# Kernel tuning notes

Measured on AMD Instinct MI355X. Metric: run time of the kernel, lower is better.

Reference implementation:

```python
import jax, jax.numpy as jnp
import numpy as np

N, FEAT, D, K, L, H, NCLS = 4096, 512, 64, 100, 3, 8, 2
EPS = 1e-15

def _ln(x, g, b, eps=1e-6):
    m = x.mean(-1, keepdims=True)
    v = x.var(-1, keepdims=True)
    return (x - m) * jax.lax.rsqrt(v + eps) * g + b


def setup_inputs():
    key = jax.random.key(0)
    ks = jax.random.split(key, 12)
    w = lambda k, shape: jax.random.normal(k, shape, jnp.float32) * 0.02
    return {
        "node_feat": jax.random.normal(ks[0], (1, N, FEAT), jnp.float32),
        "adj": jax.random.uniform(ks[1], (1, N, N), jnp.float32),
        "conv_w": w(ks[2], (FEAT, D)), "conv_b": jnp.zeros((D,), jnp.float32),
        "bn_g": jnp.ones((D,), jnp.float32), "bn_b": jnp.zeros((D,), jnp.float32),
        "pool_w": w(ks[3], (D, K)), "pool_b": jnp.zeros((K,), jnp.float32),
        "cls_token": jnp.zeros((1, 1, D), jnp.float32),
        "ln1_g": jnp.ones((L, D), jnp.float32), "ln1_b": jnp.zeros((L, D), jnp.float32),
        "qkv_w": w(ks[4], (L, D, 3 * D)), "qkv_b": jnp.zeros((L, 3 * D), jnp.float32),
        "proj_w": w(ks[5], (L, D, D)), "proj_b": jnp.zeros((L, D), jnp.float32),
        "ln2_g": jnp.ones((L, D), jnp.float32), "ln2_b": jnp.zeros((L, D), jnp.float32),
        "fc1_w": w(ks[6], (L, D, 4 * D)), "fc1_b": jnp.zeros((L, 4 * D), jnp.float32),
        "fc2_w": w(ks[7], (L, 4 * D, D)), "fc2_b": jnp.zeros((L, D), jnp.float32),
        "norm_g": jnp.ones((D,), jnp.float32), "norm_b": jnp.zeros((D,), jnp.float32),
        "head_w": w(ks[8], (D, NCLS)), "head_b": jnp.zeros((NCLS,), jnp.float32),
    }


def _forward(node_feat, adj, conv_w, conv_b, bn_g, bn_b, pool_w, pool_b, cls_token,
             ln1_g, ln1_b, qkv_w, qkv_b, proj_w, proj_b, ln2_g, ln2_b,
             fc1_w, fc1_b, fc2_w, fc2_b, norm_g, norm_b, head_w, head_b):
    x = node_feat  # mask is all ones -> X = mask*X is a no-op
    # --- GCNBlock: propagate + self loop + linear + BatchNorm(train stats) + L2 norm ---
    y = jnp.matmul(adj, x) + x                 # [1,N,F]
    y = y @ conv_w + conv_b                    # [1,N,D]
    m = y.mean(axis=(0, 1))
    v = y.var(axis=(0, 1))
    y = (y - m) * jax.lax.rsqrt(v + 1e-5) * bn_g + bn_b
    y = y / jnp.maximum(jnp.linalg.norm(y, axis=2, keepdims=True), 1e-12)
    # --- cluster assignment ---
    s = jax.nn.softmax(y @ pool_w + pool_b, axis=-1)   # [1,N,K]
    # --- dense_mincut_pool ---
    out = jnp.einsum('bnk,bnd->bkd', s, y)             # [1,K,D]
    sa = s[0].T @ adj[0]                               # [K,N] (the torch.sparse.mm)
    out_adj = (sa @ s[0])[None]                        # [1,K,K]
    mincut_num = jnp.trace(out_adj, axis1=1, axis2=2)  # [1]
    d_flat = adj.sum(-1)                               # [1,N] degrees
    # trace(S^T diag(d) S) = sum_i d_i * ||s_i||^2
    mincut_den = jnp.sum(d_flat[0] * jnp.sum(s[0] ** 2, axis=-1))[None]
    mincut_loss = jnp.mean(-(mincut_num / mincut_den))
    ss = jnp.einsum('bnk,bnl->bkl', s, s)
    i_s = jnp.eye(K, dtype=ss.dtype)
    ortho_loss = jnp.mean(jnp.linalg.norm(
        ss / jnp.linalg.norm(ss, axis=(-1, -2), keepdims=True) - i_s / jnp.linalg.norm(i_s),
        axis=(-1, -2)))
    ind = jnp.arange(K)
    out_adj = out_adj.at[:, ind, ind].set(0.0)
    dd = jnp.sqrt(out_adj.sum(-1))[:, None] + EPS      # [1,1,K]
    out_adj = out_adj / dd / jnp.swapaxes(dd, 1, 2)    # (returned by pool; unused downstream)
    # --- transformer over [cls] + K cluster tokens ---
    t = jnp.concatenate([jnp.broadcast_to(cls_token, (1, 1, D)), out], axis=1)  # [1,K+1,D]
    hd = D // H
    scale = hd ** -0.5
    for l in range(L):
        h = _ln(t, ln1_g[l], ln1_b[l])
        qkv = h @ qkv_w[l] + qkv_b[l]
        q, k, vv = jnp.split(qkv, 3, axis=-1)
        sp = lambda a: a.reshape(1, -1, H, hd).transpose(0, 2, 1, 3)
        q, k, vv = sp(q), sp(k), sp(vv)
        att = jax.nn.softmax(jnp.einsum('bhqd,bhkd->bhqk', q, k) * scale, axis=-1)
        o = jnp.einsum('bhqk,bhkd->bhqd', att, vv).transpose(0, 2, 1, 3).reshape(1, -1, D)
        t = t + (o @ proj_w[l] + proj_b[l])
        h = _ln(t, ln2_g[l], ln2_b[l])
        t = t + (jax.nn.gelu(h @ fc1_w[l] + fc1_b[l], approximate=False) @ fc2_w[l] + fc2_b[l])
    t = _ln(t, norm_g, norm_b)
    logits = t[:, 0] @ head_w + head_b                 # [1,NCLS]
    return logits, mincut_loss, ortho_loss


def reference(node_feat, adj, conv_w, conv_b, bn_g, bn_b, pool_w, pool_b, cls_token,
              ln1_g, ln1_b, qkv_w, qkv_b, proj_w, proj_b, ln2_g, ln2_b,
              fc1_w, fc1_b, fc2_w, fc2_b, norm_g, norm_b, head_w, head_b):
    return _forward(node_feat, adj, conv_w, conv_b, bn_g, bn_b, pool_w, pool_b, cls_token,
                    ln1_g, ln1_b, qkv_w, qkv_b, proj_w, proj_b, ln2_g, ln2_b,
                    fc1_w, fc1_b, fc2_w, fc2_b, norm_g, norm_b, head_w, head_b)
```

## Files before the change

kernel.cpp:

```cpp
#include <hip/hip_runtime.h>
#include <hip/hip_bf16.h>
#include <math.h>

#define NN   4096
#define FEAT 512
#define DIM  64
#define KC   100
#define LL   3

#define OFF_DFLAT   0
#define OFF_CHSUM   4096
#define OFF_CHSQ    4160
#define ZERO_FLOATS 4224
#define OFF_XW      4224
#define OFF_XWPART  (OFF_XW + NN*DIM)
#define OFF_GPART   OFF_XWPART
#define OFF_YPART   (OFF_XWPART + 8*NN*DIM)
#define OFF_Y0      (OFF_YPART + 8*NN*DIM)
#define OFF_TBUF    (OFF_Y0 + NN*DIM)
#define OFF_QKV     (OFF_TBUF + 101*DIM)
#define OFF_SS      (OFF_QKV + 101*192)
#define OFF_DENP    (OFF_SS + KC*KC)
#define OFF_NUMP    (OFF_DENP + 1024)
#define OFF_SB16    (OFF_NUMP + 1024)
#define OFF_STB16   (OFF_SB16 + NN*128/2)
#define OFF_YNT16   (OFF_STB16 + NN*128/2)
#define OFF_XWT16   (OFF_YNT16 + NN*DIM/2)

typedef __attribute__((ext_vector_type(8))) short bfrag;
typedef __attribute__((ext_vector_type(4))) float ffrag;

__device__ __forceinline__ unsigned short f2bf(float f) {
    union { float f; unsigned u; } v; v.f = f;
    return (unsigned short)((v.u + 0x7FFFu + ((v.u >> 16) & 1u)) >> 16);
}
__device__ __forceinline__ float bf2f(unsigned short u) {
    union { unsigned u; float f; } v; v.u = (unsigned)u << 16; return v.f;
}
__device__ __forceinline__ unsigned int pk2(float a, float b) {
    __hip_bfloat162 h = __float22bfloat162_rn(make_float2(a, b));
    return *(unsigned int*)&h;
}

__device__ __forceinline__ float wsum(float v) {
#pragma unroll
    for (int o = 32; o > 0; o >>= 1) v += __shfl_xor(v, o, 64);
    return v;
}
__device__ __forceinline__ float wmax(float v) {
#pragma unroll
    for (int o = 32; o > 0; o >>= 1) v = fmaxf(v, __shfl_xor(v, o, 64));
    return v;
}
__device__ __forceinline__ float hsum32(float v) {
#pragma unroll
    for (int o = 16; o > 0; o >>= 1) v += __shfl_xor(v, o, 64);
    return v;
}
__device__ __forceinline__ float hmax32(float v) {
#pragma unroll
    for (int o = 16; o > 0; o >>= 1) v = fmaxf(v, __shfl_xor(v, o, 64));
    return v;
}

template<int KDIM>
__global__ __launch_bounds__(256) void mm64(const float* __restrict__ A,
                                            const float* __restrict__ B,
                                            float* __restrict__ outp) {
    __shared__ float a_sh[64 * 68];
    __shared__ float b_sh[64 * 68];
    const int t  = threadIdx.x;
    const int rb = blockIdx.x;
    const int kspan = KDIM / gridDim.y;
    const int k0 = blockIdx.y * kspan;
    const int cg = t & 15, rg = t >> 4;
    const int srow = t >> 2, sq = t & 3;
    float4 acc[4];
#pragma unroll
    for (int i = 0; i < 4; ++i) acc[i] = make_float4(0.f, 0.f, 0.f, 0.f);
    const float* arow = A + (size_t)(rb * 64 + srow) * KDIM + k0;
    const float* brow = B + (size_t)(k0 + srow) * DIM;
    for (int kt = 0; kt < kspan; kt += 64) {
#pragma unroll
        for (int k = 0; k < 4; ++k) {
            const int j = sq * 4 + 16 * k;
            *(float4*)&a_sh[srow * 68 + j] = *(const float4*)(arow + kt + j);
            *(float4*)&b_sh[srow * 68 + j] = *(const float4*)(brow + (size_t)kt * DIM + j);
        }
        __syncthreads();
#pragma unroll 4
        for (int jj = 0; jj < 64; jj += 4) {
            const float4 w0 = *(float4*)&b_sh[(jj + 0) * 68 + 4 * cg];
            const float4 w1 = *(float4*)&b_sh[(jj + 1) * 68 + 4 * cg];
            const float4 w2 = *(float4*)&b_sh[(jj + 2) * 68 + 4 * cg];
            const float4 w3 = *(float4*)&b_sh[(jj + 3) * 68 + 4 * cg];
#pragma unroll
            for (int i = 0; i < 4; ++i) {
                const float4 av = *(float4*)&a_sh[(4 * rg + i) * 68 + jj];
                acc[i].x += av.x * w0.x + av.y * w1.x + av.z * w2.x + av.w * w3.x;
                acc[i].y += av.x * w0.y + av.y * w1.y + av.z * w2.y + av.w * w3.y;
                acc[i].z += av.x * w0.z + av.y * w1.z + av.z * w2.z + av.w * w3.z;
                acc[i].w += av.x * w0.w + av.y * w1.w + av.z * w2.w + av.w * w3.w;
            }
        }
        __syncthreads();
    }
    const int M = gridDim.x * 64;
    float* op = outp + (size_t)blockIdx.y * M * DIM;
#pragma unroll
    for (int i = 0; i < 4; ++i)
        *(float4*)&op[(size_t)(rb * 64 + 4 * rg + i) * DIM + 4 * cg] = acc[i];
}

__global__ __launch_bounds__(256) void xwred2(const float* __restrict__ part,
                                              float* __restrict__ xw,
                                              unsigned short* __restrict__ xwT) {
    __shared__ unsigned short tl[64 * 17];
    const int t = threadIdx.x, b = blockIdx.x;
    const int nb = t >> 4, d0 = (t & 15) * 4;
    const size_t e = ((size_t)(b * 16 + nb)) * 64 + d0;
    float4 v = *(const float4*)(part + e);
#pragma unroll
    for (int s = 1; s < 8; ++s) {
        const float4 u = *(const float4*)(part + (size_t)s * NN * DIM + e);
        v.x += u.x; v.y += u.y; v.z += u.z; v.w += u.w;
    }
    *(float4*)(xw + e) = v;
    tl[(d0 + 0) * 17 + nb] = f2bf(v.x);
    tl[(d0 + 1) * 17 + nb] = f2bf(v.y);
    tl[(d0 + 2) * 17 + nb] = f2bf(v.z);
    tl[(d0 + 3) * 17 + nb] = f2bf(v.w);
    __syncthreads();
    const int d = t >> 2, c = (t & 3) * 4;
    ushort4 o;
    o.x = tl[d * 17 + c + 0]; o.y = tl[d * 17 + c + 1];
    o.z = tl[d * 17 + c + 2]; o.w = tl[d * 17 + c + 3];
    *(ushort4*)(xwT + (size_t)d * NN + b * 16 + c) = o;
}

__global__ __launch_bounds__(256) void gemmA(const float* __restrict__ adj,
                                             const unsigned short* __restrict__ xwT,
                                             float* __restrict__ ypart,
                                             float* __restrict__ dflat) {
    __shared__ __align__(16) unsigned short a_sh[32 * 72];
    __shared__ __align__(16) unsigned short b_sh[64 * 72];
    const int t  = threadIdx.x;
    const int rb = blockIdx.x;
    const int k0 = blockIdx.y * 512;
    const int w = t >> 6, lane = t & 63;
    const int m = lane & 15, q = lane >> 4;
    const int ih = w & 1, jh = w >> 1;
    const int srow = t >> 3, sq = t & 7;
    const int bn = t >> 2, bc = t & 3;
    ffrag acc[2];
    acc[0] = (ffrag){0.f, 0.f, 0.f, 0.f};
    acc[1] = (ffrag){0.f, 0.f, 0.f, 0.f};
    float dacc = 0.f;
    const float* abase = adj + (size_t)(rb * 32 + srow) * NN + k0;
    const unsigned short* bbase = xwT + (size_t)bn * NN + k0;
    for (int kt = 0; kt < 512; kt += 64) {
#pragma unroll
        for (int k = 0; k < 2; ++k) {
            const int p = sq + 8 * k;
            const float4 v = *(const float4*)(abase + kt + 4 * p);
            dacc += v.x + v.y + v.z + v.w;
            *(uint2*)(a_sh + srow * 72 + 4 * p) = make_uint2(pk2(v.x, v.y), pk2(v.z, v.w));
        }
#pragma unroll
        for (int k = 0; k < 2; ++k) {
            const int c2 = bc + 4 * k;
            *(bfrag*)(b_sh + bn * 72 + c2 * 8) = *(const bfrag*)(bbase + kt + c2 * 8);
        }
        __syncthreads();
#pragma unroll
        for (int ks = 0; ks < 2; ++ks) {
            const bfrag af = *(const bfrag*)(a_sh + (ih * 16 + m) * 72 + ks * 32 + q * 8);
#pragma unroll
            for (int jj = 0; jj < 2; ++jj) {
                const bfrag bf = *(const bfrag*)(b_sh + ((jh * 2 + jj) * 16 + m) * 72 + ks * 32 + q * 8);
                acc[jj] = __builtin_amdgcn_mfma_f32_16x16x32_bf16(af, bf, acc[jj], 0, 0, 0);
            }
        }
        __syncthreads();
    }
    float* op = ypart + (size_t)blockIdx.y * NN * DIM;
#pragma unroll
    for (int jj = 0; jj < 2; ++jj)
#pragma unroll
        for (int r = 0; r < 4; ++r)
            op[(size_t)(rb * 32 + ih * 16 + q * 4 + r) * DIM + jh * 32 + jj * 16 + m] = acc[jj][r];
    dacc += __shfl_down(dacc, 1, 64);
    dacc += __shfl_down(dacc, 2, 64);
    dacc += __shfl_down(dacc, 4, 64);
    if (sq == 0) atomicAdd(&dflat[rb * 32 + srow], dacc);
}

__global__ __launch_bounds__(256) void spmmT(const float* __restrict__ adj,
                                             const unsigned short* __restrict__ ST,
                                             const unsigned short* __restrict__ Sb16,
                                             float* __restrict__ nump) {
    __shared__ __align__(16) unsigned short a_sh[32 * 72];
    __shared__ __align__(16) unsigned short s_sh[128 * 72];
    __shared__ float red[4];
    const int t  = threadIdx.x;
    const int rb = blockIdx.x;
    const int k0 = blockIdx.y * 512;
    const int w = t >> 6, lane = t & 63;
    const int m = lane & 15, q = lane >> 4;
    const int rh = w & 1, ch = w >> 1;
    const int srow = t >> 3, sq = t & 7;
    const int sn = t >> 1, sc = t & 1;
    ffrag acc[4];
#pragma unroll
    for (int j = 0; j < 4; ++j) acc[j] = (ffrag){0.f, 0.f, 0.f, 0.f};
    const float* abase = adj + (size_t)(rb * 32 + srow) * NN + k0;
    const unsigned short* sbase = ST + (size_t)sn * NN + k0;
    for (int kt = 0; kt < 512; kt += 64) {
#pragma unroll
        for (int k = 0; k < 2; ++k) {
            const int p = sq + 8 * k;
            const float4 v = *(const float4*)(abase + kt + 4 * p);
            *(uint2*)(a_sh + srow * 72 + 4 * p) = make_uint2(pk2(v.x, v.y), pk2(v.z, v.w));
        }
#pragma unroll
        for (int k = 0; k < 4; ++k) {
            const int c2 = sc + 2 * k;
            *(bfrag*)(s_sh + sn * 72 + c2 * 8) = *(const bfrag*)(sbase + kt + c2 * 8);
        }
        __syncthreads();
#pragma unroll
        for (int ks = 0; ks < 2; ++ks) {
            const bfrag af = *(const bfrag*)(a_sh + (rh * 16 + m) * 72 + ks * 32 + q * 8);
#pragma unroll
            for (int j = 0; j < 4; ++j) {
                const bfrag bf = *(const bfrag*)(s_sh + ((ch * 4 + j) * 16 + m) * 72 + ks * 32 + q * 8);
                acc[j] = __builtin_amdgcn_mfma_f32_16x16x32_bf16(af, bf, acc[j], 0, 0, 0);
            }
        }
        __syncthreads();
    }
    float local = 0.f;
#pragma unroll
    for (int j = 0; j < 4; ++j)
#pragma unroll
        for (int r = 0; r < 4; ++r) {
            const int row = rb * 32 + rh * 16 + q * 4 + r;
            const int col = ch * 64 + j * 16 + m;
            local += acc[j][r] * bf2f(Sb16[(size_t)row * 128 + col]);
        }
    local = wsum(local);
    if (lane == 0) red[w] = local;
    __syncthreads();
    if (t == 0) nump[blockIdx.y * 128 + blockIdx.x] = red[0] + red[1] + red[2] + red[3];
}

__global__ __launch_bounds__(256) void bnstat(const float* __restrict__ ypart,
                                              const float* __restrict__ xw,
                                              const float* __restrict__ conv_b,
                                              float* __restrict__ Y0,
                                              float* __restrict__ chsum,
                                              float* __restrict__ chsq) {
    __shared__ float ssum[64], ssq[64];
    const int t = threadIdx.x;
    if (t < 64) { ssum[t] = 0.f; ssq[t] = 0.f; }
    __syncthreads();
    const int tid = blockIdx.x * 256 + t;
    const size_t e = (size_t)tid * 4;
    const int c0 = (int)(e & 63);
    float4 v = *(const float4*)(xw + e);
#pragma unroll
    for (int s = 0; s < 8; ++s) {
        const float4 u = *(const float4*)(ypart + (size_t)s * NN * DIM + e);
        v.x += u.x; v.y += u.y; v.z += u.z; v.w += u.w;
    }
    const float4 b = *(const float4*)(conv_b + c0);
    v.x += b.x; v.y += b.y; v.z += b.z; v.w += b.w;
    *(float4*)(Y0 + e) = v;
    atomicAdd(&ssum[c0 + 0], v.x); atomicAdd(&ssum[c0 + 1], v.y);
    atomicAdd(&ssum[c0 + 2], v.z); atomicAdd(&ssum[c0 + 3], v.w);
    atomicAdd(&ssq[c0 + 0], v.x * v.x); atomicAdd(&ssq[c0 + 1], v.y * v.y);
    atomicAdd(&ssq[c0 + 2], v.z * v.z); atomicAdd(&ssq[c0 + 3], v.w * v.w);
    __syncthreads();
    if (t < 64) { atomicAdd(&chsum[t], ssum[t]); atomicAdd(&chsq[t], ssq[t]); }
}

__global__ __launch_bounds__(256) void rowsk(const float* __restrict__ Y0,
                                             const float* __restrict__ bn_g,
                                             const float* __restrict__ bn_b,
                                             const float* __restrict__ chsum,
                                             const float* __restrict__ chsq,
                                             const float* __restrict__ pool_w,
                                             const float* __restrict__ pool_b,
                                             const float* __restrict__ dflat,
                                             unsigned short* __restrict__ YnT,
                                             unsigned short* __restrict__ Sb16,
                                             float* __restrict__ denp) {
    __shared__ float scale_sh[64], shift_sh[64];
    __shared__ float yn_sh[4][64];
    __shared__ float4 pw4[16 * 104];
    __shared__ float denw[4];
    const int t = threadIdx.x;
    if (t < 64) {
        const float mn  = chsum[t] * (1.f / 4096.f);
        const float var = chsq[t] * (1.f / 4096.f) - mn * mn;
        const float sc  = bn_g[t] * rsqrtf(var + 1e-5f);
        scale_sh[t] = sc;
        shift_sh[t] = bn_b[t] - mn * sc;
    }
    for (int idx = t; idx < 16 * KC; idx += 256) {
        const int dq = idx / KC, k = idx - dq * KC;
        pw4[dq * 104 + k] = make_float4(pool_w[(4 * dq + 0) * KC + k],
                                        pool_w[(4 * dq + 1) * KC + k],
                                        pool_w[(4 * dq + 2) * KC + k],
                                        pool_w[(4 * dq + 3) * KC + k]);
    }
    __syncthreads();
    const int w = t >> 6, lane = t & 63;
    const int row = blockIdx.x * 4 + w;
    float v = Y0[(size_t)row * 64 + lane] * scale_sh[lane] + shift_sh[lane];
    const float nrm = fmaxf(sqrtf(wsum(v * v)), 1e-12f);
    const float yn = v / nrm;
    yn_sh[w][lane] = yn;
    __syncthreads();
    YnT[(size_t)(t >> 2) * NN + blockIdx.x * 4 + (t & 3)] = f2bf(yn_sh[t & 3][t >> 2]);
    const bool v2 = (lane + 64) < KC;
    const int j2 = v2 ? (lane + 64) : 0;
    float L1 = pool_b[lane];
    float L2 = pool_b[j2];
#pragma unroll
    for (int dq = 0; dq < 16; ++dq) {
        const float4 yv = *(const float4*)&yn_sh[w][4 * dq];
        const float4 w1 = pw4[dq * 104 + lane];
        L1 += yv.x * w1.x + yv.y * w1.y + yv.z * w1.z + yv.w * w1.w;
        const float4 w2 = pw4[dq * 104 + j2];
        L2 += yv.x * w2.x + yv.y * w2.y + yv.z * w2.z + yv.w * w2.w;
    }
    const float mx = wmax(fmaxf(L1, v2 ? L2 : -1e30f));
    const float e1 = expf(L1 - mx);
    const float e2 = v2 ? expf(L2 - mx) : 0.f;
    const float inv = 1.f / wsum(e1 + e2);
    const float s1 = e1 * inv, s2 = e2 * inv;
    Sb16[(size_t)row * 128 + lane] = f2bf(s1);
    Sb16[(size_t)row * 128 + 64 + lane] = f2bf(s2);
    const float c = wsum(s1 * s1 + s2 * s2);
    if (lane == 0) denw[w] = dflat[row] * c;
    __syncthreads();
    if (t == 0) denp[blockIdx.x] = denw[0] + denw[1] + denw[2] + denw[3];
}

__global__ __launch_bounds__(256) void transpS(const unsigned short* __restrict__ Sb,
                                               unsigned short* __restrict__ ST) {
    __shared__ __align__(16) unsigned short tl[128 * 72];
    const int t = threadIdx.x, b = blockIdx.x;
#pragma unroll
    for (int p = 0; p < 4; ++p) {
        const int n = (t >> 4) + 16 * p, c = t & 15;
        const bfrag v = *(const bfrag*)(Sb + (size_t)(b * 64 + n) * 128 + c * 8);
        const unsigned short* pv = (const unsigned short*)&v;
#pragma unroll
        for (int u = 0; u < 8; ++u) tl[(c * 8 + u) * 72 + n] = pv[u];
    }
    __syncthreads();
#pragma unroll
    for (int p = 0; p < 4; ++p) {
        const int r = (t >> 3) + 32 * p, c = t & 7;
        *(bfrag*)(ST + (size_t)r * NN + b * 64 + c * 8) = *(const bfrag*)(tl + r * 72 + c * 8);
    }
}

__global__ __launch_bounds__(256) void gram(const unsigned short* __restrict__ ST,
                                            const unsigned short* __restrict__ YnT,
                                            float* __restrict__ gpart) {
    __shared__ __align__(16) unsigned short a_sh[128 * 72];
    __shared__ __align__(16) unsigned short b_sh[192 * 72];
    const int t = threadIdx.x;
    const int k0 = blockIdx.x * 64;
    const int w = t >> 6, lane = t & 63;
    const int m = lane & 15, q = lane >> 4;
#pragma unroll
    for (int p = 0; p < 4; ++p) {
        const int n = (t >> 3) + 32 * p, c = t & 7;
        *(bfrag*)(a_sh + n * 72 + c * 8) = *(const bfrag*)(ST + (size_t)n * NN + k0 + c * 8);
    }
#pragma unroll
    for (int p = 0; p < 6; ++p) {
        const int n = (t >> 3) + 32 * p, c = t & 7;
        const unsigned short* src = (n < 64) ? (YnT + (size_t)n * NN + k0 + c * 8)
                                             : (ST + (size_t)(n - 64) * NN + k0 + c * 8);
        *(bfrag*)(b_sh + n * 72 + c * 8) = *(const bfrag*)src;
    }
    __syncthreads();
    ffrag acc[2][12];
#pragma unroll
    for (int i = 0; i < 2; ++i)
#pragma unroll
        for (int j = 0; j < 12; ++j) acc[i][j] = (ffrag){0.f, 0.f, 0.f, 0.f};
#pragma unroll
    for (int ks = 0; ks < 2; ++ks) {
        const bfrag af0 = *(const bfrag*)(a_sh + (w * 32 +  0 + m) * 72 + ks * 32 + q * 8);
        const bfrag af1 = *(const bfrag*)(a_sh + (w * 32 + 16 + m) * 72 + ks * 32 + q * 8);
#pragma unroll
        for (int j = 0; j < 12; ++j) {
            const bfrag bf = *(const bfrag*)(b_sh + (j * 16 + m) * 72 + ks * 32 + q * 8);
            acc[0][j] = __builtin_amdgcn_mfma_f32_16x16x32_bf16(af0, bf, acc[0][j], 0, 0, 0);
            acc[1][j] = __builtin_amdgcn_mfma_f32_16x16x32_bf16(af1, bf, acc[1][j], 0, 0, 0);
        }
    }
    float* op = gpart + (size_t)blockIdx.x * 128 * 192;
#pragma unroll
    for (int i = 0; i < 2; ++i)
#pragma unroll
        for (int j = 0; j < 12; ++j)
#pragma unroll
            for (int r = 0; r < 4; ++r)
                op[(size_t)(w * 32 + i * 16 + q * 4 + r) * 192 + j * 16 + m] = acc[i][j][r];
}

__global__ __launch_bounds__(256) void gramred(const float* __restrict__ gpart,
                                               const float* __restrict__ cls,
                                               float* __restrict__ tbuf,
                                               float* __restrict__ ss) {
    const int tid = blockIdx.x * 256 + threadIdx.x;
    if (tid < 128 * 192) {
        const int row = tid / 192, col = tid - row * 192;
        float v = 0.f;
        for (int s = 0; s < 64; ++s) v += gpart[(size_t)s * 128 * 192 + tid];
        if (row < KC) {
            if (col < 64) tbuf[(row + 1) * 64 + col] = v;
            else if (col < 164) ss[row * KC + (col - 64)] = v;
        }
    } else if (tid < 128 * 192 + 64) {
        const int c = tid - 128 * 192;
        tbuf[c] = cls[c];
    }
}

__global__ __launch_bounds__(256) void attnA(const float* __restrict__ tbuf,
                                             const float* __restrict__ g1,
                                             const float* __restrict__ b1,
                                             const float* __restrict__ qw,
                                             const float* __restrict__ qb,
                                             float* __restrict__ qkvb, int l) {
    __shared__ float wl[64 * 192];
    __shared__ float hs[64];
    const int t = threadIdx.x, tok = blockIdx.x;
    const float* wsrc = qw + (size_t)l * 64 * 192;
#pragma unroll
    for (int p = 0; p < 12; ++p) {
        const int idx = t + 256 * p;
        *(float4*)&wl[idx * 4] = *(const float4*)(wsrc + idx * 4);
    }
    if (t < 64) {
        const float x = tbuf[tok * 64 + t];
        const float m = wsum(x) * (1.f / 64.f);
        const float var = wsum(x * x) * (1.f / 64.f) - m * m;
        hs[t] = (x - m) * rsqrtf(var + 1e-6f) * g1[l * 64 + t] + b1[l * 64 + t];
    }
    __syncthreads();
    if (t < 192) {
        float a = qb[l * 192 + t];
#pragma unroll 8
        for (int e = 0; e < 64; ++e)
            a += hs[e] * wl[e * 192 + t];
        qkvb[tok * 192 + t] = a;
    }
}

__global__ __launch_bounds__(256) void attnB(float* __restrict__ tbuf,
                                             const float* __restrict__ qkvb,
                                             const float* __restrict__ pw,
                                             const float* __restrict__ pb,
                                             const float* __restrict__ g2,
                                             const float* __restrict__ b2,
                                             const float* __restrict__ w1,
                                             const float* __restrict__ bb1,
                                             const float* __restrict__ w2,
                                             const float* __restrict__ bb2, int l) {
    __shared__ float big[13332];
    __shared__ float sc[8 * 104];
    __shared__ float q_l[64], osh[64], h2sh[64], gsh[256];
    const int t = threadIdx.x, qtok = blockIdx.x;
    float t_old = 0.f;
    if (t < 64) t_old = tbuf[qtok * 64 + t];
#pragma unroll
    for (int p = 0; p < 13; ++p) {
        const int idx = t + 256 * p;
        if (idx < 101 * 32) {
            const int k = idx >> 5, c = idx & 31;
            *(float4*)&big[k * 132 + c * 4] = *(const float4*)(qkvb + k * 192 + 64 + c * 4);
        }
    }
    if (t < 16) *(float4*)&q_l[t * 4] = *(const float4*)(qkvb + qtok * 192 + t * 4);
    __syncthreads();
    const float scale = 0.35355339059327373f;
#pragma unroll
    for (int p = 0; p < 4; ++p) {
        const int idx = t + 256 * p;
        if (idx < 808) {
            const int h = idx / 101, k = idx - h * 101;
            float s = 0.f;
#pragma unroll
            for (int d = 0; d < 8; ++d)
                s += q_l[h * 8 + d] * big[k * 132 + h * 8 + d];
            sc[h * 104 + k] = s * scale;
        }
    }
    __syncthreads();
    {
        const int w = t >> 6;
        const int h = w * 2 + ((t >> 5) & 1);
        const int lft = t & 31;
        float v[4];
#pragma unroll
        for (int g = 0; g < 4; ++g) {
            const int k = lft + 32 * g;
            v[g] = (k < 101) ? sc[h * 104 + k] : -1e30f;
        }
        float m = fmaxf(fmaxf(v[0], v[1]), fmaxf(v[2], v[3]));
        m = hmax32(m);
        float s = 0.f;
#pragma unroll
        for (int g = 0; g < 4; ++g) { v[g] = expf(v[g] - m); s += v[g]; }
        s = hsum32(s);
        const float inv = 1.f / s;
#pragma unroll
        for (int g = 0; g < 4; ++g) {
            const int k = lft + 32 * g;
            if (k < 101) sc[h * 104 + k] = v[g] * inv;
        }
    }
    __syncthreads();
    if (t < 64) {
        const int h = t >> 3, d = t & 7;
        float o = 0.f;
        for (int k = 0; k < 101; ++k)
            o += sc[h * 104 + k] * big[k * 132 + 64 + h * 8 + d];
        osh[h * 8 + d] = o;
    }
    __syncthreads();
#pragma unroll
    for (int p = 0; p < 4; ++p) {
        const int idx = t + 256 * p;
        *(float4*)&big[idx * 4] = *(const float4*)(pw + (size_t)l * 4096 + idx * 4);
    }
    __syncthreads();
    float t1 = 0.f;
    if (t < 64) {
        float pr = pb[l * 64 + t];
#pragma unroll 8
        for (int e = 0; e < 64; ++e)
            pr += osh[e] * big[e * 64 + t];
        t1 = t_old + pr;
        const float m = wsum(t1) * (1.f / 64.f);
        const float var = wsum(t1 * t1) * (1.f / 64.f) - m * m;
        h2sh[t] = (t1 - m) * rsqrtf(var + 1e-6f) * g2[l * 64 + t] + b2[l * 64 + t];
    }
    __syncthreads();
    for (int ch = 0; ch < 2; ++ch) {
#pragma unroll
        for (int p = 0; p < 8; ++p) {
            const int idx = t + 256 * p;
            const int e = idx >> 5, c = idx & 31;
            *(float4*)&big[e * 128 + c * 4] =
                *(const float4*)(w1 + (size_t)l * 16384 + e * 256 + ch * 128 + c * 4);
        }
        __syncthreads();
        if (t < 128) {
            float a = bb1[l * 256 + ch * 128 + t];
#pragma unroll 8
            for (int e = 0; e < 64; ++e)
                a += h2sh[e] * big[e * 128 + t];
            gsh[ch * 128 + t] = 0.5f * a * (1.f + erff(a * 0.70710678118654752f));
        }
        __syncthreads();
    }
    float a2 = (t < 64) ? bb2[l * 64 + t] : 0.f;
    for (int ch = 0; ch < 2; ++ch) {
#pragma unroll
        for (int p = 0; p < 8; ++p) {
            const int idx = t + 256 * p;
            *(float4*)&big[idx * 4] =
                *(const float4*)(w2 + (size_t)l * 16384 + ch * 8192 + idx * 4);
        }
        __syncthreads();
        if (t < 64) {
#pragma unroll 8
            for (int er = 0; er < 128; ++er)
                a2 += gsh[ch * 128 + er] * big[er * 64 + t];
        }
        __syncthreads();
    }
    if (t < 64) tbuf[qtok * 64 + t] = t1 + a2;
}

__global__ __launch_bounds__(256) void finalk(const float* __restrict__ tbuf,
                                              const float* __restrict__ ng,
                                              const float* __restrict__ nb,
                                              const float* __restrict__ hw,
                                              const float* __restrict__ hb,
                                              const float* __restrict__ ss,
                                              const float* __restrict__ denp,
                                              const float* __restrict__ nump,
                                              float* __restrict__ out) {
    __shared__ float f0[64];
    __shared__ float red[256];
    __shared__ float fro_sh, den_sh, num_sh;
    const int t = threadIdx.x;
    if (t < 64) {
        const float x = tbuf[t];
        const float m = wsum(x) * (1.f / 64.f);
        const float var = wsum(x * x) * (1.f / 64.f) - m * m;
        f0[t] = (x - m) * rsqrtf(var + 1e-6f) * ng[t] + nb[t];
    }
    red[t] = denp[t] + denp[t + 256] + denp[t + 512] + denp[t + 768];
    __syncthreads();
    for (int s = 128; s > 0; s >>= 1) { if (t < s) red[t] += red[t + s]; __syncthreads(); }
    if (t == 0) den_sh = red[0];
    __syncthreads();
    red[t] = nump[t] + nump[t + 256] + nump[t + 512] + nump[t + 768];
    __syncthreads();
    for (int s = 128; s > 0; s >>= 1) { if (t < s) red[t] += red[t + s]; __syncthreads(); }
    if (t == 0) num_sh = red[0];
    __syncthreads();
    if (t < 2) {
        float a = hb[t];
        for (int d = 0; d < 64; ++d) a += f0[d] * hw[d * 2 + t];
        out[t] = a;
    }
    if (t == 2) out[2] = -(num_sh / den_sh);
    float s1 = 0.f;
    for (int idx = t; idx < KC * KC; idx += 256) { const float v = ss[idx]; s1 += v * v; }
    __syncthreads();
    red[t] = s1;
    __syncthreads();
    for (int s = 128; s > 0; s >>= 1) { if (t < s) red[t] += red[t + s]; __syncthreads(); }
    if (t == 0) fro_sh = sqrtf(red[0]);
    __syncthreads();
    const float inv = 1.f / fro_sh;
    float s2 = 0.f;
    for (int idx = t; idx < KC * KC; idx += 256) {
        float v = ss[idx] * inv;
        if (idx % 101 == 0) v -= 0.1f;
        s2 += v * v;
    }
    __syncthreads();
    red[t] = s2;
    __syncthreads();
    for (int s = 128; s > 0; s >>= 1) { if (t < s) red[t] += red[t + s]; __syncthreads(); }
    if (t == 0) out[3] = sqrtf(red[0]);
}

extern "C" void kernel_launch(void* const* d_in, const int* in_sizes, int n_in,
                              void* d_out, int out_size, void* d_ws, size_t ws_size,
                              hipStream_t stream) {
    (void)in_sizes; (void)n_in; (void)out_size; (void)ws_size;
    const float* x      = (const float*)d_in[0];
    const float* adj    = (const float*)d_in[1];
    const float* conv_w = (const float*)d_in[2];
    const float* conv_b = (const float*)d_in[3];
    const float* bn_g   = (const float*)d_in[4];
    const float* bn_b   = (const float*)d_in[5];
    const float* pool_w = (const float*)d_in[6];
    const float* pool_b = (const float*)d_in[7];
    const float* cls    = (const float*)d_in[8];
    const float* ln1_g  = (const float*)d_in[9];
    const float* ln1_b  = (const float*)d_in[10];
    const float* qkv_w  = (const float*)d_in[11];
    const float* qkv_b  = (const float*)d_in[12];
    const float* proj_w = (const float*)d_in[13];
    const float* proj_b = (const float*)d_in[14];
    const float* ln2_g  = (const float*)d_in[15];
    const float* ln2_b  = (const float*)d_in[16];
    const float* fc1_w  = (const float*)d_in[17];
    const float* fc1_b  = (const float*)d_in[18];
    const float* fc2_w  = (const float*)d_in[19];
    const float* fc2_b  = (const float*)d_in[20];
    const float* norm_g = (const float*)d_in[21];
    const float* norm_b = (const float*)d_in[22];
    const float* head_w = (const float*)d_in[23];
    const float* head_b = (const float*)d_in[24];
    float* ws  = (float*)d_ws;
    float* out = (float*)d_out;
    unsigned short* Sb16  = (unsigned short*)(ws + OFF_SB16);
    unsigned short* STb16 = (unsigned short*)(ws + OFF_STB16);
    unsigned short* YnT16 = (unsigned short*)(ws + OFF_YNT16);
    unsigned short* xwT16 = (unsigned short*)(ws + OFF_XWT16);

    hipMemsetAsync(ws, 0, ZERO_FLOATS * sizeof(float), stream);
    mm64<FEAT><<<dim3(64, 8), 256, 0, stream>>>(x, conv_w, ws + OFF_XWPART);
    xwred2<<<256, 256, 0, stream>>>(ws + OFF_XWPART, ws + OFF_XW, xwT16);
    gemmA<<<dim3(128, 8), 256, 0, stream>>>(adj, xwT16, ws + OFF_YPART, ws + OFF_DFLAT);
    bnstat<<<256, 256, 0, stream>>>(ws + OFF_YPART, ws + OFF_XW, conv_b,
                                    ws + OFF_Y0, ws + OFF_CHSUM, ws + OFF_CHSQ);
    rowsk<<<1024, 256, 0, stream>>>(ws + OFF_Y0, bn_g, bn_b, ws + OFF_CHSUM, ws + OFF_CHSQ,
                                    pool_w, pool_b, ws + OFF_DFLAT,
                                    YnT16, Sb16, ws + OFF_DENP);
    transpS<<<64, 256, 0, stream>>>(Sb16, STb16);
    spmmT<<<dim3(128, 8), 256, 0, stream>>>(adj, STb16, Sb16, ws + OFF_NUMP);
    gram<<<64, 256, 0, stream>>>(STb16, YnT16, ws + OFF_GPART);
    gramred<<<97, 256, 0, stream>>>(ws + OFF_GPART, cls, ws + OFF_TBUF, ws + OFF_SS);
    for (int l = 0; l < LL; ++l) {
        attnA<<<101, 256, 0, stream>>>(ws + OFF_TBUF, ln1_g, ln1_b, qkv_w, qkv_b, ws + OFF_QKV, l);
        attnB<<<101, 256, 0, stream>>>(ws + OFF_TBUF, ws + OFF_QKV, proj_w, proj_b,
                                       ln2_g, ln2_b, fc1_w, fc1_b, fc2_w, fc2_b, l);
    }
    finalk<<<1, 256, 0, stream>>>(ws + OFF_TBUF, norm_g, norm_b, head_w, head_b,
                                  ws + OFF_SS, ws + OFF_DENP, ws + OFF_NUMP, out);
}
```

Before: 299.9 us.

## Fuse X·W with its reduction and workspace zeroing; merge attention kernels per layer

Replaces the split-K mm64 plus xwred2 reduction and the workspace memset with one xwk kernel. It computes X·conv_w per 16-row block, writes fp32 and a transposed bf16 copy, and zeroes the accumulators. The attnA/attnB pair per layer becomes one attnL kernel with 512 threads and dynamic LDS. Each block recomputes LN1 and QKV for all 101 tokens locally, and layers ping-pong between two token buffers. This removes several launches and global round-trips, but adds about 101x redundant QKV computation per layer and a much larger LDS footprint per block.

```diff
diff --git a/kernel.cpp b/kernel.cpp
--- a/kernel.cpp
+++ b/kernel.cpp
@@ -13,13 +13,12 @@
 #define OFF_CHSQ    4160
 #define ZERO_FLOATS 4224
 #define OFF_XW      4224
-#define OFF_XWPART  (OFF_XW + NN*DIM)
-#define OFF_GPART   OFF_XWPART
-#define OFF_YPART   (OFF_XWPART + 8*NN*DIM)
-#define OFF_Y0      (OFF_YPART + 8*NN*DIM)
+#define OFF_YPART   (OFF_XW + NN*DIM)
+#define OFF_GPART   (OFF_YPART + 8*NN*DIM)
+#define OFF_Y0      (OFF_GPART + 64*128*192)
 #define OFF_TBUF    (OFF_Y0 + NN*DIM)
-#define OFF_QKV     (OFF_TBUF + 101*DIM)
-#define OFF_SS      (OFF_QKV + 101*192)
+#define OFF_TBUF2   (OFF_TBUF + 101*DIM)
+#define OFF_SS      (OFF_TBUF2 + 101*DIM)
 #define OFF_DENP    (OFF_SS + KC*KC)
 #define OFF_NUMP    (OFF_DENP + 1024)
 #define OFF_SB16    (OFF_NUMP + 1024)
@@ -27,6 +26,11 @@
 #define OFF_YNT16   (OFF_STB16 + NN*128/2)
 #define OFF_XWT16   (OFF_YNT16 + NN*DIM/2)
 
+#define AL_QKV   0
+#define AL_WBUF  19496
+#define AL_XS    (AL_WBUF + 12288)
+#define AL_TOTAL (AL_XS + 6568)
+
 typedef __attribute__((ext_vector_type(8))) short bfrag;
 typedef __attribute__((ext_vector_type(4))) float ffrag;
 
@@ -63,79 +67,51 @@
     return v;
 }
 
-template<int KDIM>
-__global__ __launch_bounds__(256) void mm64(const float* __restrict__ A,
-                                            const float* __restrict__ B,
-                                            float* __restrict__ outp) {
-    __shared__ float a_sh[64 * 68];
+__global__ __launch_bounds__(256) void xwk(const float* __restrict__ x,
+                                           const float* __restrict__ B,
+                                           float* __restrict__ xw,
+                                           unsigned short* __restrict__ xwT,
+                                           float* __restrict__ zws) {
+    __shared__ float a_sh[16 * 68];
     __shared__ float b_sh[64 * 68];
-    const int t  = threadIdx.x;
-    const int rb = blockIdx.x;
-    const int kspan = KDIM / gridDim.y;
-    const int k0 = blockIdx.y * kspan;
-    const int cg = t & 15, rg = t >> 4;
-    const int srow = t >> 2, sq = t & 3;
-    float4 acc[4];
-#pragma unroll
-    for (int i = 0; i < 4; ++i) acc[i] = make_float4(0.f, 0.f, 0.f, 0.f);
-    const float* arow = A + (size_t)(rb * 64 + srow) * KDIM + k0;
-    const float* brow = B + (size_t)(k0 + srow) * DIM;
-    for (int kt = 0; kt < kspan; kt += 64) {
-#pragma unroll
-        for (int k = 0; k < 4; ++k) {
-            const int j = sq * 4 + 16 * k;
-            *(float4*)&a_sh[srow * 68 + j] = *(const float4*)(arow + kt + j);
-            *(float4*)&b_sh[srow * 68 + j] = *(const float4*)(brow + (size_t)kt * DIM + j);
+    __shared__ unsigned short tl[64 * 17];
+    const int t = threadIdx.x, rb = blockIdx.x;
+    if (rb < 17) {
+        const int zi = rb * 256 + t;
+        if (zi < ZERO_FLOATS) zws[zi] = 0.f;
+    }
+    const int r = t >> 4, cg = (t & 15) * 4;
+    float4 acc = make_float4(0.f, 0.f, 0.f, 0.f);
+    for (int kt = 0; kt < FEAT; kt += 64) {
+        *(float4*)&a_sh[(t >> 4) * 68 + (t & 15) * 4] =
+            *(const float4*)(x + (size_t)(rb * 16 + (t >> 4)) * FEAT + kt + (t & 15) * 4);
+#pragma unroll
+        for (int p = 0; p < 4; ++p) {
+            const int idx = t + 256 * p;
+            const int kr = idx >> 4, c4 = (idx & 15) * 4;
+            *(float4*)&b_sh[kr * 68 + c4] = *(const float4*)(B + (size_t)(kt + kr) * DIM + c4);
         }
         __syncthreads();
-#pragma unroll 4
-        for (int jj = 0; jj < 64; jj += 4) {
-            const float4 w0 = *(float4*)&b_sh[(jj + 0) * 68 + 4 * cg];
-            const float4 w1 = *(float4*)&b_sh[(jj + 1) * 68 + 4 * cg];
-            const float4 w2 = *(float4*)&b_sh[(jj + 2) * 68 + 4 * cg];
-            const float4 w3 = *(float4*)&b_sh[(jj + 3) * 68 + 4 * cg];
-#pragma unroll
-            for (int i = 0; i < 4; ++i) {
-                const float4 av = *(float4*)&a_sh[(4 * rg + i) * 68 + jj];
-                acc[i].x += av.x * w0.x + av.y * w1.x + av.z * w2.x + av.w * w3.x;
-                acc[i].y += av.x * w0.y + av.y * w1.y + av.z * w2.y + av.w * w3.y;
-                acc[i].z += av.x * w0.z + av.y * w1.z + av.z * w2.z + av.w * w3.z;
-                acc[i].w += av.x * w0.w + av.y * w1.w + av.z * w2.w + av.w * w3.w;
-            }
+#pragma unroll 8
+        for (int k = 0; k < 64; ++k) {
+            const float av = a_sh[r * 68 + k];
+            const float4 bv = *(float4*)&b_sh[k * 68 + cg];
+            acc.x += av * bv.x; acc.y += av * bv.y;
+            acc.z += av * bv.z; acc.w += av * bv.w;
         }
         __syncthreads();
     }
-    const int M = gridDim.x * 64;
-    float* op = outp + (size_t)blockIdx.y * M * DIM;
-#pragma unroll
-    for (int i = 0; i < 4; ++i)
-        *(float4*)&op[(size_t)(rb * 64 + 4 * rg + i) * DIM + 4 * cg] = acc[i];
-}
-
-__global__ __launch_bounds__(256) void xwred2(const float* __restrict__ part,
-                                              float* __restrict__ xw,
-                                              unsigned short* __restrict__ xwT) {
-    __shared__ unsigned short tl[64 * 17];
-    const int t = threadIdx.x, b = blockIdx.x;
-    const int nb = t >> 4, d0 = (t & 15) * 4;
-    const size_t e = ((size_t)(b * 16 + nb)) * 64 + d0;
-    float4 v = *(const float4*)(part + e);
-#pragma unroll
-    for (int s = 1; s < 8; ++s) {
-        const float4 u = *(const float4*)(part + (size_t)s * NN * DIM + e);
-        v.x += u.x; v.y += u.y; v.z += u.z; v.w += u.w;
-    }
-    *(float4*)(xw + e) = v;
-    tl[(d0 + 0) * 17 + nb] = f2bf(v.x);
-    tl[(d0 + 1) * 17 + nb] = f2bf(v.y);
-    tl[(d0 + 2) * 17 + nb] = f2bf(v.z);
-    tl[(d0 + 3) * 17 + nb] = f2bf(v.w);
+    *(float4*)&xw[(size_t)(rb * 16 + r) * DIM + cg] = acc;
+    tl[(cg + 0) * 17 + r] = f2bf(acc.x);
+    tl[(cg + 1) * 17 + r] = f2bf(acc.y);
+    tl[(cg + 2) * 17 + r] = f2bf(acc.z);
+    tl[(cg + 3) * 17 + r] = f2bf(acc.w);
     __syncthreads();
     const int d = t >> 2, c = (t & 3) * 4;
     ushort4 o;
     o.x = tl[d * 17 + c + 0]; o.y = tl[d * 17 + c + 1];
     o.z = tl[d * 17 + c + 2]; o.w = tl[d * 17 + c + 3];
-    *(ushort4*)(xwT + (size_t)d * NN + b * 16 + c) = o;
+    *(ushort4*)(xwT + (size_t)d * NN + rb * 16 + c) = o;
 }
 
 __global__ __launch_bounds__(256) void gemmA(const float* __restrict__ adj,
@@ -209,7 +185,7 @@
     const int m = lane & 15, q = lane >> 4;
     const int rh = w & 1, ch = w >> 1;
     const int srow = t >> 3, sq = t & 7;
-    const int sn = t >> 1, sc = t & 1;
+    const int sn = t >> 1, sc2 = t & 1;
     ffrag acc[4];
 #pragma unroll
     for (int j = 0; j < 4; ++j) acc[j] = (ffrag){0.f, 0.f, 0.f, 0.f};
@@ -224,7 +200,7 @@
         }
 #pragma unroll
         for (int k = 0; k < 4; ++k) {
-            const int c2 = sc + 2 * k;
+            const int c2 = sc2 + 2 * k;
             *(bfrag*)(s_sh + sn * 72 + c2 * 8) = *(const bfrag*)(sbase + kt + c2 * 8);
         }
         __syncthreads();
@@ -435,39 +411,12 @@
     }
 }
 
-__global__ __launch_bounds__(256) void attnA(const float* __restrict__ tbuf,
+__global__ __launch_bounds__(512) void attnL(const float* __restrict__ tin,
+                                             float* __restrict__ tout,
                                              const float* __restrict__ g1,
                                              const float* __restrict__ b1,
                                              const float* __restrict__ qw,
                                              const float* __restrict__ qb,
-                                             float* __restrict__ qkvb, int l) {
-    __shared__ float wl[64 * 192];
-    __shared__ float hs[64];
-    const int t = threadIdx.x, tok = blockIdx.x;
-    const float* wsrc = qw + (size_t)l * 64 * 192;
-#pragma unroll
-    for (int p = 0; p < 12; ++p) {
-        const int idx = t + 256 * p;
-        *(float4*)&wl[idx * 4] = *(const float4*)(wsrc + idx * 4);
-    }
-    if (t < 64) {
-        const float x = tbuf[tok * 64 + t];
-        const float m = wsum(x) * (1.f / 64.f);
-        const float var = wsum(x * x) * (1.f / 64.f) - m * m;
-        hs[t] = (x - m) * rsqrtf(var + 1e-6f) * g1[l * 64 + t] + b1[l * 64 + t];
-    }
-    __syncthreads();
-    if (t < 192) {
-        float a = qb[l * 192 + t];
-#pragma unroll 8
-        for (int e = 0; e < 64; ++e)
-            a += hs[e] * wl[e * 192 + t];
-        qkvb[tok * 192 + t] = a;
-    }
-}
-
-__global__ __launch_bounds__(256) void attnB(float* __restrict__ tbuf,
-                                             const float* __restrict__ qkvb,
                                              const float* __restrict__ pw,
                                              const float* __restrict__ pb,
                                              const float* __restrict__ g2,
@@ -475,40 +424,69 @@
                                              const float* __restrict__ w1,
                                              const float* __restrict__ bb1,
                                              const float* __restrict__ w2,
-                                             const float* __restrict__ bb2, int l) {
-    __shared__ float big[13332];
+                                             const float* __restrict__ bb2,
+                                             int l) {
+    extern __shared__ float lds[];
+    float* qkvs = lds + AL_QKV;
+    float* wbuf = lds + AL_WBUF;
+    float* xs   = lds + AL_XS;
     __shared__ float sc[8 * 104];
-    __shared__ float q_l[64], osh[64], h2sh[64], gsh[256];
+    __shared__ float osh[64], h2sh[64], gsh[256];
+    __shared__ float m_s[101], s_s[101];
     const int t = threadIdx.x, qtok = blockIdx.x;
-    float t_old = 0.f;
-    if (t < 64) t_old = tbuf[qtok * 64 + t];
+#pragma unroll
+    for (int p = 0; p < 6; ++p) {
+        const int idx = t + 512 * p;
+        ((float4*)wbuf)[idx] = ((const float4*)(qw + (size_t)l * 12288))[idx];
+    }
 #pragma unroll
     for (int p = 0; p < 13; ++p) {
-        const int idx = t + 256 * p;
-        if (idx < 101 * 32) {
-            const int k = idx >> 5, c = idx & 31;
-            *(float4*)&big[k * 132 + c * 4] = *(const float4*)(qkvb + k * 192 + 64 + c * 4);
-        }
-    }
-    if (t < 16) *(float4*)&q_l[t * 4] = *(const float4*)(qkvb + qtok * 192 + t * 4);
+        const int idx = t + 512 * p;
+        if (idx < 101 * 64) xs[(idx >> 6) * 65 + (idx & 63)] = tin[idx];
+    }
+    __syncthreads();
+    if (t < 101) {
+        float s = 0.f, sq = 0.f;
+        for (int e = 0; e < 64; ++e) { const float v = xs[t * 65 + e]; s += v; sq += v * v; }
+        const float m = s * (1.f / 64.f);
+        m_s[t] = m;
+        s_s[t] = rsqrtf(sq * (1.f / 64.f) - m * m + 1e-6f);
+    }
+    __syncthreads();
+#pragma unroll
+    for (int p = 0; p < 13; ++p) {
+        const int idx = t + 512 * p;
+        if (idx < 101 * 64) {
+            const int tok = idx >> 6, e = idx & 63;
+            xs[tok * 65 + e] = (xs[tok * 65 + e] - m_s[tok]) * s_s[tok] * g1[l * 64 + e]
+                               + b1[l * 64 + e];
+        }
+    }
+    __syncthreads();
+    for (int g = t; g < 101 * 48; g += 512) {
+        const int tok = g / 48, j4 = (g - tok * 48) * 4;
+        float4 a = *(const float4*)(qb + (size_t)l * 192 + j4);
+        for (int e = 0; e < 64; ++e) {
+            const float hv = xs[tok * 65 + e];
+            const float4 w4 = *(float4*)&wbuf[e * 192 + j4];
+            a.x += hv * w4.x; a.y += hv * w4.y; a.z += hv * w4.z; a.w += hv * w4.w;
+        }
+        qkvs[tok * 193 + j4 + 0] = a.x; qkvs[tok * 193 + j4 + 1] = a.y;
+        qkvs[tok * 193 + j4 + 2] = a.z; qkvs[tok * 193 + j4 + 3] = a.w;
+    }
     __syncthreads();
     const float scale = 0.35355339059327373f;
-#pragma unroll
-    for (int p = 0; p < 4; ++p) {
-        const int idx = t + 256 * p;
-        if (idx < 808) {
-            const int h = idx / 101, k = idx - h * 101;
-            float s = 0.f;
-#pragma unroll
-            for (int d = 0; d < 8; ++d)
-                s += q_l[h * 8 + d] * big[k * 132 + h * 8 + d];
-            sc[h * 104 + k] = s * scale;
-        }
-    }
-    __syncthreads();
-    {
-        const int w = t >> 6;
-        const int h = w * 2 + ((t >> 5) & 1);
+    for (int idx = t; idx < 808; idx += 512) {
+        const int h = idx / 101, k = idx - h * 101;
+        float s = 0.f;
+#pragma unroll
+        for (int d = 0; d < 8; ++d)
+            s += qkvs[qtok * 193 + h * 8 + d] * qkvs[k * 193 + 64 + h * 8 + d];
+        sc[h * 104 + k] = s * scale;
+    }
+    __syncthreads();
+    if (t < 256) {
+        const int h = (t >> 5);
         const int lft = t & 31;
         float v[4];
 #pragma unroll
@@ -531,17 +509,17 @@
     }
     __syncthreads();
     if (t < 64) {
-        const int h = t >> 3, d = t & 7;
+        const int h = t >> 3;
         float o = 0.f;
         for (int k = 0; k < 101; ++k)
-            o += sc[h * 104 + k] * big[k * 132 + 64 + h * 8 + d];
-        osh[h * 8 + d] = o;
-    }
-    __syncthreads();
-#pragma unroll
-    for (int p = 0; p < 4; ++p) {
-        const int idx = t + 256 * p;
-        *(float4*)&big[idx * 4] = *(const float4*)(pw + (size_t)l * 4096 + idx * 4);
+            o += sc[h * 104 + k] * qkvs[k * 193 + 128 + t];
+        osh[t] = o;
+    }
+    __syncthreads();
+#pragma unroll
+    for (int p = 0; p < 2; ++p) {
+        const int idx = t + 512 * p;
+        ((float4*)wbuf)[idx] = ((const float4*)(pw + (size_t)l * 4096))[idx];
     }
     __syncthreads();
     float t1 = 0.f;
@@ -549,48 +527,40 @@
         float pr = pb[l * 64 + t];
 #pragma unroll 8
         for (int e = 0; e < 64; ++e)
-            pr += osh[e] * big[e * 64 + t];
-        t1 = t_old + pr;
+            pr += osh[e] * wbuf[e * 64 + t];
+        t1 = tin[qtok * 64 + t] + pr;
         const float m = wsum(t1) * (1.f / 64.f);
         const float var = wsum(t1 * t1) * (1.f / 64.f) - m * m;
         h2sh[t] = (t1 - m) * rsqrtf(var + 1e-6f) * g2[l * 64 + t] + b2[l * 64 + t];
     }
     __syncthreads();
-    for (int ch = 0; ch < 2; ++ch) {
-#pragma unroll
-        for (int p = 0; p < 8; ++p) {
-            const int idx = t + 256 * p;
-            const int e = idx >> 5, c = idx & 31;
-            *(float4*)&big[e * 128 + c * 4] =
-                *(const float4*)(w1 + (size_t)l * 16384 + e * 256 + ch * 128 + c * 4);
-        }
-        __syncthreads();
-        if (t < 128) {
-            float a = bb1[l * 256 + ch * 128 + t];
+#pragma unroll
+    for (int p = 0; p < 8; ++p) {
+        const int idx = t + 512 * p;
+        ((float4*)qkvs)[idx] = ((const float4*)(w1 + (size_t)l * 16384))[idx];
+    }
+    __syncthreads();
+    if (t < 256) {
+        float a = bb1[l * 256 + t];
 #pragma unroll 8
-            for (int e = 0; e < 64; ++e)
-                a += h2sh[e] * big[e * 128 + t];
-            gsh[ch * 128 + t] = 0.5f * a * (1.f + erff(a * 0.70710678118654752f));
-        }
-        __syncthreads();
-    }
-    float a2 = (t < 64) ? bb2[l * 64 + t] : 0.f;
-    for (int ch = 0; ch < 2; ++ch) {
-#pragma unroll
-        for (int p = 0; p < 8; ++p) {
-            const int idx = t + 256 * p;
-            *(float4*)&big[idx * 4] =
-                *(const float4*)(w2 + (size_t)l * 16384 + ch * 8192 + idx * 4);
-        }
-        __syncthreads();
-        if (t < 64) {
+        for (int e = 0; e < 64; ++e)
+            a += h2sh[e] * qkvs[e * 256 + t];
+        gsh[t] = 0.5f * a * (1.f + erff(a * 0.70710678118654752f));
+    }
+    __syncthreads();
+#pragma unroll
+    for (int p = 0; p < 8; ++p) {
+        const int idx = t + 512 * p;
+        ((float4*)qkvs)[idx] = ((const float4*)(w2 + (size_t)l * 16384))[idx];
+    }
+    __syncthreads();
+    if (t < 64) {
+        float a2 = bb2[l * 64 + t];
 #pragma unroll 8
-            for (int er = 0; er < 128; ++er)
-                a2 += gsh[ch * 128 + er] * big[er * 64 + t];
-        }
-        __syncthreads();
-    }
-    if (t < 64) tbuf[qtok * 64 + t] = t1 + a2;
+        for (int e = 0; e < 256; ++e)
+            a2 += gsh[e] * qkvs[e * 64 + t];
+        tout[qtok * 64 + t] = t1 + a2;
+    }
 }
 
 __global__ __launch_bounds__(256) void finalk(const float* __restrict__ tbuf,
@@ -686,9 +656,15 @@
     unsigned short* YnT16 = (unsigned short*)(ws + OFF_YNT16);
     unsigned short* xwT16 = (unsigned short*)(ws + OFF_XWT16);
 
-    hipMemsetAsync(ws, 0, ZERO_FLOATS * sizeof(float), stream);
-    mm64<FEAT><<<dim3(64, 8), 256, 0, stream>>>(x, conv_w, ws + OFF_XWPART);
-    xwred2<<<256, 256, 0, stream>>>(ws + OFF_XWPART, ws + OFF_XW, xwT16);
+    static bool attr_done = false;
+    if (!attr_done) {
+        hipFuncSetAttribute((const void*)attnL,
+                            hipFuncAttributeMaxDynamicSharedMemorySize,
+                            AL_TOTAL * (int)sizeof(float));
+        attr_done = true;
+    }
+
+    xwk<<<256, 256, 0, stream>>>(x, conv_w, ws + OFF_XW, xwT16, ws);
     gemmA<<<dim3(128, 8), 256, 0, stream>>>(adj, xwT16, ws + OFF_YPART, ws + OFF_DFLAT);
     bnstat<<<256, 256, 0, stream>>>(ws + OFF_YPART, ws + OFF_XW, conv_b,
                                     ws + OFF_Y0, ws + OFF_CHSUM, ws + OFF_CHSQ);
@@ -699,11 +675,15 @@
     spmmT<<<dim3(128, 8), 256, 0, stream>>>(adj, STb16, Sb16, ws + OFF_NUMP);
     gram<<<64, 256, 0, stream>>>(STb16, YnT16, ws + OFF_GPART);
     gramred<<<97, 256, 0, stream>>>(ws + OFF_GPART, cls, ws + OFF_TBUF, ws + OFF_SS);
-    for (int l = 0; l < LL; ++l) {
-        attnA<<<101, 256, 0, stream>>>(ws + OFF_TBUF, ln1_g, ln1_b, qkv_w, qkv_b, ws + OFF_QKV, l);
-        attnB<<<101, 256, 0, stream>>>(ws + OFF_TBUF, ws + OFF_QKV, proj_w, proj_b,
-                                       ln2_g, ln2_b, fc1_w, fc1_b, fc2_w, fc2_b, l);
-    }
-    finalk<<<1, 256, 0, stream>>>(ws + OFF_TBUF, norm_g, norm_b, head_w, head_b,
+    const size_t dynLds = AL_TOTAL * sizeof(float);
+    float* tb0 = ws + OFF_TBUF;
+    float* tb1 = ws + OFF_TBUF2;
+    attnL<<<101, 512, dynLds, stream>>>(tb0, tb1, ln1_g, ln1_b, qkv_w, qkv_b, proj_w, proj_b,
+                                        ln2_g, ln2_b, fc1_w, fc1_b, fc2_w, fc2_b, 0);
+    attnL<<<101, 512, dynLds, stream>>>(tb1, tb0, ln1_g, ln1_b, qkv_w, qkv_b, proj_w, proj_b,
+                                        ln2_g, ln2_b, fc1_w, fc1_b, fc2_w, fc2_b, 1);
+    attnL<<<101, 512, dynLds, stream>>>(tb0, tb1, ln1_g, ln1_b, qkv_w, qkv_b, proj_w, proj_b,
+                                        ln2_g, ln2_b, fc1_w, fc1_b, fc2_w, fc2_b, 2);
+    finalk<<<1, 256, 0, stream>>>(tb1, norm_g, norm_b, head_w, head_b,
                                   ws + OFF_SS, ws + OFF_DENP, ws + OFF_NUMP, out);
 }
```

Result: slower. 329.3 us (+9.8%).
